# Optimization experiments

Hardware: AMD Instinct MI355X
Metric: run time of the kernel (lower is better)

Reference implementation:

```python
import jax, jax.numpy as jnp
import numpy as np

N_NODES = 100000
N_EDGES = 1600000
IN_DIM, H1, H2, OUT_DIM = 128, 64, 64, 64


def _glorot(key, shape):
    fan_in, fan_out = shape
    lim = np.sqrt(6.0 / (fan_in + fan_out)).astype(np.float32)
    return jax.random.uniform(key, shape, jnp.float32, -lim, lim)


def setup_inputs() -> dict:
    key = jax.random.key(0)
    ks = jax.random.split(key, 8)
    x = jax.random.normal(ks[0], (N_NODES, IN_DIM), jnp.float32)
    edge_index = jax.random.randint(ks[1], (2, N_EDGES), 0, N_NODES, jnp.int64)
    W1 = _glorot(ks[2], (IN_DIM, H1))
    b1 = jnp.zeros((H1,), jnp.float32)
    W2 = _glorot(ks[3], (H1, H2))
    b2 = jnp.zeros((H2,), jnp.float32)
    Wfc = _glorot(ks[4], (H2, OUT_DIM))
    bfc = jnp.zeros((OUT_DIM,), jnp.float32)
    return {"x": x, "W1": W1, "b1": b1, "W2": W2, "b2": b2,
            "Wfc": Wfc, "bfc": bfc, "edge_index": edge_index}


def _gcn_conv(x, src, dst, dinv, W, b, n_nodes):
    # PyG GCNConv: h = D^{-1/2} (A + I) D^{-1/2} (x W) + b
    h = x @ W                                   # [N, out]
    norm = dinv[src] * dinv[dst]                # [E'] edge weights
    msg = norm[:, None] * h[src]                # gather + scale, [E', out]
    agg = jax.ops.segment_sum(msg, dst, num_segments=n_nodes)
    return agg + b


def reference(x, W1, b1, W2, b2, Wfc, bfc, edge_index):
    n = x.shape[0]
    loop = jnp.arange(n, dtype=edge_index.dtype)
    src = jnp.concatenate([edge_index[0], loop])   # self-loops appended
    dst = jnp.concatenate([edge_index[1], loop])
    deg = jnp.zeros((n,), x.dtype).at[dst].add(1.0)  # degree incl. self-loop
    dinv = jax.lax.rsqrt(deg)

    h = jax.nn.relu(_gcn_conv(x, src, dst, dinv, W1, b1, n))
    h = jax.nn.relu(_gcn_conv(h, src, dst, dinv, W2, b2, n))
    embedding = h
    logits = h @ Wfc + bfc
    return embedding, logits
```

## Files before the change

kernel.cpp:

```cpp
#include <hip/hip_runtime.h>
#include <hip/hip_bf16.h>


constexpr int IN_DIM  = 128;
constexpr int HDIM    = 64;
constexpr int NBLK_A  = 256;
constexpr int BSH     = 8;
constexpr int MAXNB   = 512;
constexpr int PADSLK  = 1792;

__device__ __forceinline__ float bf2f(unsigned int u) {
    return __uint_as_float(u << 16);
}
__device__ __forceinline__ unsigned short f2bf_bits(float f) {
    __hip_bfloat16 b = __float2bfloat16(f);
    return *(unsigned short*)&b;
}


__global__ void binA_count(const int* __restrict__ dst, int* __restrict__ histg,
                           int E, int NB, int chunk) {
    __shared__ int h[MAXNB];
    for (int i = threadIdx.x; i < NB; i += 256) h[i] = 0;
    __syncthreads();
    int beg = blockIdx.x * chunk;
    int end = min(E, beg + chunk);
    for (int e = beg + threadIdx.x; e < end; e += 256)
        atomicAdd(&h[dst[e] >> BSH], 1);
    __syncthreads();
    for (int i = threadIdx.x; i < NB; i += 256)
        histg[i * NBLK_A + blockIdx.x] = h[i];
}

__global__ void binA_scanblocks(int* __restrict__ histg, int* __restrict__ btot) {
    __shared__ int sm[NBLK_A];
    int tid = threadIdx.x;
    int v = histg[blockIdx.x * NBLK_A + tid];
    sm[tid] = v;
    __syncthreads();
    for (int off = 1; off < NBLK_A; off <<= 1) {
        int t = (tid >= off) ? sm[tid - off] : 0;
        __syncthreads();
        sm[tid] += t;
        __syncthreads();
    }
    histg[blockIdx.x * NBLK_A + tid] = sm[tid] - v;
    if (tid == NBLK_A - 1) btot[blockIdx.x] = sm[tid];
}

__global__ void binA_scanbuckets(const int* __restrict__ btot, int* __restrict__ bucketbase,
                                 int NB) {
    __shared__ int sm[MAXNB];
    int tid = threadIdx.x;
    int v = (tid < NB) ? btot[tid] : 0;
    sm[tid] = v;
    __syncthreads();
    for (int off = 1; off < MAXNB; off <<= 1) {
        int t = (tid >= off) ? sm[tid - off] : 0;
        __syncthreads();
        sm[tid] += t;
        __syncthreads();
    }
    if (tid < NB) bucketbase[tid] = sm[tid] - v;
    if (tid == MAXNB - 1) bucketbase[NB] = sm[tid];
}

__global__ void binA_scatter(const int* __restrict__ src, const int* __restrict__ dst,
                             const int* __restrict__ histg, const int* __restrict__ bucketbase,
                             int* __restrict__ staging, int E, int NB, int chunk) {
    __shared__ int cur[MAXNB];
    for (int i = threadIdx.x; i < NB; i += 256)
        cur[i] = bucketbase[i] + histg[i * NBLK_A + blockIdx.x];
    __syncthreads();
    int beg = blockIdx.x * chunk;
    int end = min(E, beg + chunk);
    for (int e = beg + threadIdx.x; e < end; e += 256) {
        int s = src[e];
        int d = dst[e];
        int pos = atomicAdd(&cur[d >> BSH], 1);
        staging[pos] = (s << BSH) | (d & 255);
    }
}

__global__ void binB_finalize(const int* __restrict__ staging, const int* __restrict__ bucketbase,
                              int2* __restrict__ rows, int* __restrict__ esrc,
                              float* __restrict__ dinv, unsigned int* __restrict__ hp_rowN,
                              int N, int NB) {
    __shared__ int cnt[256], sm[256], cur[256];
    int tid = threadIdx.x;
    int b = blockIdx.x;
    int node0 = b << BSH;
    int nloc = min(256, N - node0);
    int ebeg = bucketbase[b], eend = bucketbase[b + 1];
    int ebegP = ebeg + b * PADSLK;
    cnt[tid] = 0;
    __syncthreads();
    for (int e = ebeg + tid; e < eend; e += 256)
        atomicAdd(&cnt[staging[e] & 255], 1);
    __syncthreads();
    int v = cnt[tid];
    int pv = (v + 7) & ~7;
    sm[tid] = pv;
    __syncthreads();
    for (int off = 1; off < 256; off <<= 1) {
        int t = (tid >= off) ? sm[tid - off] : 0;
        __syncthreads();
        sm[tid] += t;
        __syncthreads();
    }
    int excl = sm[tid] - pv;
    cur[tid] = excl;
    __syncthreads();
    if (tid < nloc) {
        rows[node0 + tid] = make_int2(ebegP + excl, ebegP + excl + pv);
        dinv[node0 + tid] = rsqrtf((float)v + 1.0f);
        for (int q = v; q < pv; ++q)
            esrc[ebegP + excl + q] = N;
    }
    if (b == 0 && tid < 32) hp_rowN[tid] = 0u;
    for (int e = ebeg + tid; e < eend; e += 256) {
        int p = staging[e];
        int pos = ebegP + atomicAdd(&cur[p & 255], 1);
        esrc[pos] = p >> BSH;
    }
}


template<int K, bool IBF16, bool SCALE, bool BIAS, bool OBF16>
__device__ __forceinline__ void gemm_body(
        const void* __restrict__ Xv, const float* __restrict__ W,
        const float* __restrict__ bias, const float* __restrict__ dinv,
        void* __restrict__ Yv, int n) {
    constexpr int KC = 32;
    constexpr int XSTR = 132;
    __shared__ float Xt[KC * XSTR];
    __shared__ float Ws[KC * 64];
    const int tid = threadIdx.x;
    const int node0 = blockIdx.x * 128;
    const int r0 = (tid >> 4) * 8;
    const int c0 = (tid & 15) * 4;

    float acc[8][4];
#pragma unroll
    for (int a = 0; a < 8; ++a)
#pragma unroll
        for (int b = 0; b < 4; ++b) acc[a][b] = 0.f;

    for (int kc = 0; kc < K; kc += KC) {
        __syncthreads();
#pragma unroll
        for (int i = 0; i < 4; ++i) {
            int s = tid + i * 256;
            int row = s >> 3;
            int kq = s & 7;
            int grow = node0 + row;
            float4 v = make_float4(0.f, 0.f, 0.f, 0.f);
            if (grow < n) {
                if (IBF16) {
                    uint2 u = *(const uint2*)&((const unsigned short*)Xv)[(size_t)grow * K + kc + kq * 4];
                    v.x = bf2f(u.x & 0xffff); v.y = bf2f(u.x >> 16);
                    v.z = bf2f(u.y & 0xffff); v.w = bf2f(u.y >> 16);
                } else {
                    v = *(const float4*)&((const float*)Xv)[(size_t)grow * K + kc + kq * 4];
                }
            }
            Xt[(kq * 4 + 0) * XSTR + row] = v.x;
            Xt[(kq * 4 + 1) * XSTR + row] = v.y;
            Xt[(kq * 4 + 2) * XSTR + row] = v.z;
            Xt[(kq * 4 + 3) * XSTR + row] = v.w;
        }
#pragma unroll
        for (int i = 0; i < 2; ++i) {
            int s = tid + i * 256;
            *(float4*)&Ws[s * 4] = *(const float4*)&W[(size_t)kc * 64 + s * 4];
        }
        __syncthreads();
#pragma unroll
        for (int kk = 0; kk < KC; kk += 4) {
            float4 xa[4][2];
            float4 wv[4];
#pragma unroll
            for (int i = 0; i < 4; ++i) {
                xa[i][0] = *(const float4*)&Xt[(kk + i) * XSTR + r0];
                xa[i][1] = *(const float4*)&Xt[(kk + i) * XSTR + r0 + 4];
                wv[i]    = *(const float4*)&Ws[(kk + i) * 64 + c0];
            }
#pragma unroll
            for (int i = 0; i < 4; ++i) {
                const float* xp = (const float*)&xa[i][0];
                const float* wp = (const float*)&wv[i];
#pragma unroll
                for (int rr = 0; rr < 8; ++rr)
#pragma unroll
                    for (int cc = 0; cc < 4; ++cc)
                        acc[rr][cc] += xp[rr] * wp[cc];
            }
        }
    }
#pragma unroll
    for (int rr = 0; rr < 8; ++rr) {
        int node = node0 + r0 + rr;
        if (node < n) {
            float d = SCALE ? dinv[node] : 1.0f;
            float t[4];
#pragma unroll
            for (int cc = 0; cc < 4; ++cc) {
                float v = acc[rr][cc];
                if (BIAS) v += bias[c0 + cc];
                t[cc] = v * d;
            }
            if (OBF16) {
                __hip_bfloat16 vb[4];
#pragma unroll
                for (int cc = 0; cc < 4; ++cc) vb[cc] = __float2bfloat16(t[cc]);
                *(uint2*)&((__hip_bfloat16*)Yv)[(size_t)node * 64 + c0] = *(uint2*)vb;
            } else {
                *(float4*)&((float*)Yv)[(size_t)node * 64 + c0] = *(float4*)t;
            }
        }
    }
}

__global__ __launch_bounds__(256, 4) void gemm1_kernel(
        const float* X, const float* W, const float* dinv, void* Y, int n) {
    gemm_body<IN_DIM, false, true, false, true>(X, W, nullptr, dinv, Y, n);
}
__global__ __launch_bounds__(256, 4) void gemm2_kernel(
        const void* X, const float* W, const float* dinv, void* Y, int n) {
    gemm_body<HDIM, true, true, false, true>(X, W, nullptr, dinv, Y, n);
}
__global__ __launch_bounds__(256, 4) void fc_kernel(
        const float* X, const float* W, const float* bias, void* Y, int n) {
    gemm_body<HDIM, false, false, true, false>(X, W, bias, nullptr, Y, n);
}

template<bool OBF16>
__global__ __launch_bounds__(256) void agg_kernel(
        const uint4* __restrict__ hp4, const int* __restrict__ esrc,
        const int2* __restrict__ rows, const float* __restrict__ dinv,
        const float* __restrict__ bias, void* __restrict__ out, int n) {
    const int lane = threadIdx.x & 63;
    const int j = lane & 7;
    const int node = blockIdx.x * 32 + (threadIdx.x >> 6) * 8 + (lane >> 3);
    if (node >= n) return;
    const int2 be = rows[node];

    float acc[8];
    {
        uint4 u = hp4[(size_t)node * 8 + j];
        acc[0] = bf2f(u.x & 0xffff); acc[1] = bf2f(u.x >> 16);
        acc[2] = bf2f(u.y & 0xffff); acc[3] = bf2f(u.y >> 16);
        acc[4] = bf2f(u.z & 0xffff); acc[5] = bf2f(u.z >> 16);
        acc[6] = bf2f(u.w & 0xffff); acc[7] = bf2f(u.w >> 16);
    }
    for (int k = be.x; k < be.y; k += 8) {
        int s[8];
#pragma unroll
        for (int i = 0; i < 8; ++i)
            s[i] = __builtin_nontemporal_load(&esrc[k + i]);
        uint4 u[8];
#pragma unroll
        for (int i = 0; i < 8; ++i)
            u[i] = hp4[(size_t)s[i] * 8 + j];
#pragma unroll
        for (int i = 0; i < 8; ++i) {
            acc[0] += bf2f(u[i].x & 0xffff); acc[1] += bf2f(u[i].x >> 16);
            acc[2] += bf2f(u[i].y & 0xffff); acc[3] += bf2f(u[i].y >> 16);
            acc[4] += bf2f(u[i].z & 0xffff); acc[5] += bf2f(u[i].z >> 16);
            acc[6] += bf2f(u[i].w & 0xffff); acc[7] += bf2f(u[i].w >> 16);
        }
    }
    const float d = dinv[node];
    float o[8];
#pragma unroll
    for (int t = 0; t < 8; ++t)
        o[t] = fmaxf(fmaf(d, acc[t], bias[8 * j + t]), 0.f);

    if (OBF16) {
        uint4 pk;
        pk.x = (unsigned)f2bf_bits(o[0]) | ((unsigned)f2bf_bits(o[1]) << 16);
        pk.y = (unsigned)f2bf_bits(o[2]) | ((unsigned)f2bf_bits(o[3]) << 16);
        pk.z = (unsigned)f2bf_bits(o[4]) | ((unsigned)f2bf_bits(o[5]) << 16);
        pk.w = (unsigned)f2bf_bits(o[6]) | ((unsigned)f2bf_bits(o[7]) << 16);
        ((uint4*)out)[(size_t)node * 8 + j] = pk;
    } else {
        ((float4*)out)[(size_t)node * 16 + 2 * j]     = make_float4(o[0], o[1], o[2], o[3]);
        ((float4*)out)[(size_t)node * 16 + 2 * j + 1] = make_float4(o[4], o[5], o[6], o[7]);
    }
}

extern "C" void kernel_launch(void* const* d_in, const int* in_sizes, int n_in,
                              void* d_out, int out_size, void* d_ws, size_t ws_size,
                              hipStream_t stream) {
    const float* x   = (const float*)d_in[0];
    const float* W1  = (const float*)d_in[1];
    const float* b1  = (const float*)d_in[2];
    const float* W2  = (const float*)d_in[3];
    const float* b2  = (const float*)d_in[4];
    const float* Wfc = (const float*)d_in[5];
    const float* bfc = (const float*)d_in[6];
    const int*  eidx = (const int*)d_in[7];

    const int N = in_sizes[0] / IN_DIM;
    const int E = in_sizes[7] / 2;
    const int* src = eidx;
    const int* dst = eidx + E;

    const int NB    = (N + 255) >> BSH;
    const int chunk = (E + NBLK_A - 1) / NBLK_A;
    const int EP    = E + NB * PADSLK;

    int* p = (int*)d_ws;
    int2* rows = (int2*)p;           p += (size_t)2 * N + 2;
    float* dinv = (float*)p;         p += (size_t)((N + 3) & ~3);
    int* histg = p;                  p += (size_t)((NB * NBLK_A + 3) & ~3);
    int* btot = p;                   p += 512;
    int* bucketbase = p;             p += 512;
    int* esrc = p;                   p += (size_t)((EP + 3) & ~3);
    unsigned short* hp = (unsigned short*)p;   p += (size_t)(N + 1) * 32;
    unsigned short* h1 = (unsigned short*)p;   p += (size_t)N * 32;
    int* staging = (int*)hp;
    unsigned int* hp_rowN = (unsigned int*)(hp + (size_t)N * 64);

    float* emb    = (float*)d_out;
    float* logits = emb + (size_t)N * HDIM;

    binA_count<<<NBLK_A, 256, 0, stream>>>(dst, histg, E, NB, chunk);
    binA_scanblocks<<<NB, NBLK_A, 0, stream>>>(histg, btot);
    binA_scanbuckets<<<1, MAXNB, 0, stream>>>(btot, bucketbase, NB);
    binA_scatter<<<NBLK_A, 256, 0, stream>>>(src, dst, histg, bucketbase, staging, E, NB, chunk);
    binB_finalize<<<NB, 256, 0, stream>>>(staging, bucketbase, rows, esrc, dinv, hp_rowN, N, NB);

    const int gBlocks = (N + 127) / 128;
    const int aBlocks = (N + 31) / 32;

    gemm1_kernel<<<gBlocks, 256, 0, stream>>>(x, W1, dinv, hp, N);
    agg_kernel<true><<<aBlocks, 256, 0, stream>>>(
        (const uint4*)hp, esrc, rows, dinv, b1, h1, N);

    gemm2_kernel<<<gBlocks, 256, 0, stream>>>(h1, W2, dinv, hp, N);
    agg_kernel<false><<<aBlocks, 256, 0, stream>>>(
        (const uint4*)hp, esrc, rows, dinv, b2, emb, N);

    fc_kernel<<<gBlocks, 256, 0, stream>>>(emb, Wfc, bfc, logits, N);
}
```

Baseline: 315.4 us.

## Sort nodes by padded degree class to balance aggregation wavefronts

Adds three small kernels that bucket nodes by padded edge-trip count into 16 classes and build a permutation. Both aggregation kernels then process nodes in this permuted order, so the 8 nodes sharing a wavefront have similar loop trip counts and divergence is reduced. The cost is three extra launches and an indirect perm lookup. Output writes also become scattered and lose locality with the row and hp reads.

```diff
diff --git a/kernel.cpp b/kernel.cpp
--- a/kernel.cpp
+++ b/kernel.cpp
@@ -8,6 +8,7 @@
 constexpr int BSH     = 8;
 constexpr int MAXNB   = 512;
 constexpr int PADSLK  = 1792;
+constexpr int NCLASS  = 16;
 
 __device__ __forceinline__ float bf2f(unsigned int u) {
     return __uint_as_float(u << 16);
@@ -85,7 +86,7 @@
 __global__ void binB_finalize(const int* __restrict__ staging, const int* __restrict__ bucketbase,
                               int2* __restrict__ rows, int* __restrict__ esrc,
                               float* __restrict__ dinv, unsigned int* __restrict__ hp_rowN,
-                              int N, int NB) {
+                              int* __restrict__ classCnt, int N, int NB) {
     __shared__ int cnt[256], sm[256], cur[256];
     int tid = threadIdx.x;
     int b = blockIdx.x;
@@ -94,6 +95,7 @@
     int ebeg = bucketbase[b], eend = bucketbase[b + 1];
     int ebegP = ebeg + b * PADSLK;
     cnt[tid] = 0;
+    if (b == 0 && tid < NCLASS) classCnt[tid] = 0;
     __syncthreads();
     for (int e = ebeg + tid; e < eend; e += 256)
         atomicAdd(&cnt[staging[e] & 255], 1);
@@ -123,6 +125,49 @@
         int pos = ebegP + atomicAdd(&cur[p & 255], 1);
         esrc[pos] = p >> BSH;
     }
+}
+
+
+__device__ __forceinline__ int trip_class(int2 be) {
+    return min((be.y - be.x) >> 3, NCLASS - 1);
+}
+
+__global__ void classCount(const int2* __restrict__ rows, int* __restrict__ classCnt, int N) {
+    __shared__ int lc[NCLASS];
+    if (threadIdx.x < NCLASS) lc[threadIdx.x] = 0;
+    __syncthreads();
+    int i = blockIdx.x * 256 + threadIdx.x;
+    if (i < N) atomicAdd(&lc[trip_class(rows[i])], 1);
+    __syncthreads();
+    if (threadIdx.x < NCLASS) atomicAdd(&classCnt[threadIdx.x], lc[threadIdx.x]);
+}
+
+__global__ void classScan(const int* __restrict__ classCnt, int* __restrict__ classCur) {
+    if (threadIdx.x == 0) {
+        int base = 0;
+        for (int t = 0; t < NCLASS; ++t) {
+            classCur[t] = base;
+            base += classCnt[t];
+        }
+    }
+}
+
+__global__ void classAssign(const int2* __restrict__ rows, int* __restrict__ classCur,
+                            int* __restrict__ perm, int N) {
+    __shared__ int lc[NCLASS], lbase[NCLASS];
+    if (threadIdx.x < NCLASS) lc[threadIdx.x] = 0;
+    __syncthreads();
+    int i = blockIdx.x * 256 + threadIdx.x;
+    int t = -1, r = 0;
+    if (i < N) {
+        t = trip_class(rows[i]);
+        r = atomicAdd(&lc[t], 1);
+    }
+    __syncthreads();
+    if (threadIdx.x < NCLASS && lc[threadIdx.x] > 0)
+        lbase[threadIdx.x] = atomicAdd(&classCur[threadIdx.x], lc[threadIdx.x]);
+    __syncthreads();
+    if (i < N) perm[lbase[t] + r] = i;
 }
 
 
@@ -238,11 +283,13 @@
 __global__ __launch_bounds__(256) void agg_kernel(
         const uint4* __restrict__ hp4, const int* __restrict__ esrc,
         const int2* __restrict__ rows, const float* __restrict__ dinv,
-        const float* __restrict__ bias, void* __restrict__ out, int n) {
+        const float* __restrict__ bias, const int* __restrict__ perm,
+        void* __restrict__ out, int n) {
     const int lane = threadIdx.x & 63;
     const int j = lane & 7;
-    const int node = blockIdx.x * 32 + (threadIdx.x >> 6) * 8 + (lane >> 3);
-    if (node >= n) return;
+    const int idx = blockIdx.x * 32 + (threadIdx.x >> 6) * 8 + (lane >> 3);
+    if (idx >= n) return;
+    const int node = perm[idx];
     const int2 be = rows[node];
 
     float acc[8];
@@ -316,6 +363,9 @@
     int* histg = p;                  p += (size_t)((NB * NBLK_A + 3) & ~3);
     int* btot = p;                   p += 512;
     int* bucketbase = p;             p += 512;
+    int* classCnt = p;               p += NCLASS;
+    int* classCur = p;               p += NCLASS;
+    int* perm = p;                   p += (size_t)((N + 3) & ~3);
     int* esrc = p;                   p += (size_t)((EP + 3) & ~3);
     unsigned short* hp = (unsigned short*)p;   p += (size_t)(N + 1) * 32;
     unsigned short* h1 = (unsigned short*)p;   p += (size_t)N * 32;
@@ -325,22 +375,29 @@
     float* emb    = (float*)d_out;
     float* logits = emb + (size_t)N * HDIM;
 
+    const int nBlocks256 = (N + 255) / 256;
+
     binA_count<<<NBLK_A, 256, 0, stream>>>(dst, histg, E, NB, chunk);
     binA_scanblocks<<<NB, NBLK_A, 0, stream>>>(histg, btot);
     binA_scanbuckets<<<1, MAXNB, 0, stream>>>(btot, bucketbase, NB);
     binA_scatter<<<NBLK_A, 256, 0, stream>>>(src, dst, histg, bucketbase, staging, E, NB, chunk);
-    binB_finalize<<<NB, 256, 0, stream>>>(staging, bucketbase, rows, esrc, dinv, hp_rowN, N, NB);
+    binB_finalize<<<NB, 256, 0, stream>>>(staging, bucketbase, rows, esrc, dinv, hp_rowN,
+                                          classCnt, N, NB);
+
+    classCount<<<nBlocks256, 256, 0, stream>>>(rows, classCnt, N);
+    classScan<<<1, 64, 0, stream>>>(classCnt, classCur);
+    classAssign<<<nBlocks256, 256, 0, stream>>>(rows, classCur, perm, N);
 
     const int gBlocks = (N + 127) / 128;
     const int aBlocks = (N + 31) / 32;
 
     gemm1_kernel<<<gBlocks, 256, 0, stream>>>(x, W1, dinv, hp, N);
     agg_kernel<true><<<aBlocks, 256, 0, stream>>>(
-        (const uint4*)hp, esrc, rows, dinv, b1, h1, N);
+        (const uint4*)hp, esrc, rows, dinv, b1, perm, h1, N);
 
     gemm2_kernel<<<gBlocks, 256, 0, stream>>>(h1, W2, dinv, hp, N);
     agg_kernel<false><<<aBlocks, 256, 0, stream>>>(
-        (const uint4*)hp, esrc, rows, dinv, b2, emb, N);
+        (const uint4*)hp, esrc, rows, dinv, b2, perm, emb, N);
 
     fc_kernel<<<gBlocks, 256, 0, stream>>>(emb, Wfc, bfc, logits, N);
 }
```

New measurement: 338.8 us. 7.4% more time.

## Fold bucket scan into scatter/finalize, grid-stride aggregation with 16-wide unroll

Applied to the files above, without the earlier changes.

Removes the single-block bucket-scan kernel by having every scatter and finalize block recompute the 512-entry bucket prefix scan redundantly in shared memory, which saves one launch and its dependency bubble. The aggregation kernel becomes a grid-stride loop over a fixed 2048-block grid and processes edges 16 at a time with an 8-wide tail, so more gathers are in flight per node. The redundant per-block scans add shared-memory work and barriers. The fixed grid and larger unroll may lower occupancy through higher register use.

```diff
diff --git a/kernel.cpp b/kernel.cpp
--- a/kernel.cpp
+++ b/kernel.cpp
@@ -48,29 +48,30 @@
     if (tid == NBLK_A - 1) btot[blockIdx.x] = sm[tid];
 }
 
-__global__ void binA_scanbuckets(const int* __restrict__ btot, int* __restrict__ bucketbase,
-                                 int NB) {
-    __shared__ int sm[MAXNB];
+__device__ __forceinline__ void bucket_scan(const int* __restrict__ btot,
+                                            int* bb, int NB) {
     int tid = threadIdx.x;
-    int v = (tid < NB) ? btot[tid] : 0;
-    sm[tid] = v;
+    for (int i = tid; i < MAXNB; i += 256) bb[i] = (i < NB) ? btot[i] : 0;
     __syncthreads();
     for (int off = 1; off < MAXNB; off <<= 1) {
-        int t = (tid >= off) ? sm[tid - off] : 0;
-        __syncthreads();
-        sm[tid] += t;
-        __syncthreads();
-    }
-    if (tid < NB) bucketbase[tid] = sm[tid] - v;
-    if (tid == MAXNB - 1) bucketbase[NB] = sm[tid];
+        int i0 = tid, i1 = tid + 256;
+        int t0 = (i0 >= off) ? bb[i0 - off] : 0;
+        int t1 = (i1 >= off) ? bb[i1 - off] : 0;
+        __syncthreads();
+        bb[i0] += t0;
+        bb[i1] += t1;
+        __syncthreads();
+    }
 }
 
 __global__ void binA_scatter(const int* __restrict__ src, const int* __restrict__ dst,
-                             const int* __restrict__ histg, const int* __restrict__ bucketbase,
+                             const int* __restrict__ histg, const int* __restrict__ btot,
                              int* __restrict__ staging, int E, int NB, int chunk) {
+    __shared__ int bb[MAXNB];
     __shared__ int cur[MAXNB];
+    bucket_scan(btot, bb, NB);
     for (int i = threadIdx.x; i < NB; i += 256)
-        cur[i] = bucketbase[i] + histg[i * NBLK_A + blockIdx.x];
+        cur[i] = (bb[i] - btot[i]) + histg[i * NBLK_A + blockIdx.x];
     __syncthreads();
     int beg = blockIdx.x * chunk;
     int end = min(E, beg + chunk);
@@ -82,16 +83,19 @@
     }
 }
 
-__global__ void binB_finalize(const int* __restrict__ staging, const int* __restrict__ bucketbase,
+__global__ void binB_finalize(const int* __restrict__ staging, const int* __restrict__ btot,
                               int2* __restrict__ rows, int* __restrict__ esrc,
                               float* __restrict__ dinv, unsigned int* __restrict__ hp_rowN,
                               int N, int NB) {
+    __shared__ int bb[MAXNB];
     __shared__ int cnt[256], sm[256], cur[256];
     int tid = threadIdx.x;
     int b = blockIdx.x;
+    bucket_scan(btot, bb, NB);
     int node0 = b << BSH;
     int nloc = min(256, N - node0);
-    int ebeg = bucketbase[b], eend = bucketbase[b + 1];
+    int eend = bb[b];
+    int ebeg = eend - btot[b];
     int ebegP = ebeg + b * PADSLK;
     cnt[tid] = 0;
     __syncthreads();
@@ -241,51 +245,72 @@
         const float* __restrict__ bias, void* __restrict__ out, int n) {
     const int lane = threadIdx.x & 63;
     const int j = lane & 7;
-    const int node = blockIdx.x * 32 + (threadIdx.x >> 6) * 8 + (lane >> 3);
-    if (node >= n) return;
-    const int2 be = rows[node];
-
-    float acc[8];
-    {
-        uint4 u = hp4[(size_t)node * 8 + j];
-        acc[0] = bf2f(u.x & 0xffff); acc[1] = bf2f(u.x >> 16);
-        acc[2] = bf2f(u.y & 0xffff); acc[3] = bf2f(u.y >> 16);
-        acc[4] = bf2f(u.z & 0xffff); acc[5] = bf2f(u.z >> 16);
-        acc[6] = bf2f(u.w & 0xffff); acc[7] = bf2f(u.w >> 16);
-    }
-    for (int k = be.x; k < be.y; k += 8) {
-        int s[8];
-#pragma unroll
-        for (int i = 0; i < 8; ++i)
-            s[i] = __builtin_nontemporal_load(&esrc[k + i]);
-        uint4 u[8];
-#pragma unroll
-        for (int i = 0; i < 8; ++i)
-            u[i] = hp4[(size_t)s[i] * 8 + j];
-#pragma unroll
-        for (int i = 0; i < 8; ++i) {
-            acc[0] += bf2f(u[i].x & 0xffff); acc[1] += bf2f(u[i].x >> 16);
-            acc[2] += bf2f(u[i].y & 0xffff); acc[3] += bf2f(u[i].y >> 16);
-            acc[4] += bf2f(u[i].z & 0xffff); acc[5] += bf2f(u[i].z >> 16);
-            acc[6] += bf2f(u[i].w & 0xffff); acc[7] += bf2f(u[i].w >> 16);
-        }
-    }
-    const float d = dinv[node];
-    float o[8];
-#pragma unroll
-    for (int t = 0; t < 8; ++t)
-        o[t] = fmaxf(fmaf(d, acc[t], bias[8 * j + t]), 0.f);
-
-    if (OBF16) {
-        uint4 pk;
-        pk.x = (unsigned)f2bf_bits(o[0]) | ((unsigned)f2bf_bits(o[1]) << 16);
-        pk.y = (unsigned)f2bf_bits(o[2]) | ((unsigned)f2bf_bits(o[3]) << 16);
-        pk.z = (unsigned)f2bf_bits(o[4]) | ((unsigned)f2bf_bits(o[5]) << 16);
-        pk.w = (unsigned)f2bf_bits(o[6]) | ((unsigned)f2bf_bits(o[7]) << 16);
-        ((uint4*)out)[(size_t)node * 8 + j] = pk;
-    } else {
-        ((float4*)out)[(size_t)node * 16 + 2 * j]     = make_float4(o[0], o[1], o[2], o[3]);
-        ((float4*)out)[(size_t)node * 16 + 2 * j + 1] = make_float4(o[4], o[5], o[6], o[7]);
+    const int step = gridDim.x * 32;
+    for (int idx = blockIdx.x * 32 + (threadIdx.x >> 6) * 8 + (lane >> 3);
+         idx < n; idx += step) {
+        const int node = idx;
+        const int2 be = rows[node];
+
+        float acc[8];
+        {
+            uint4 u = hp4[(size_t)node * 8 + j];
+            acc[0] = bf2f(u.x & 0xffff); acc[1] = bf2f(u.x >> 16);
+            acc[2] = bf2f(u.y & 0xffff); acc[3] = bf2f(u.y >> 16);
+            acc[4] = bf2f(u.z & 0xffff); acc[5] = bf2f(u.z >> 16);
+            acc[6] = bf2f(u.w & 0xffff); acc[7] = bf2f(u.w >> 16);
+        }
+        int k = be.x;
+        for (; k + 16 <= be.y; k += 16) {
+            int s[16];
+#pragma unroll
+            for (int i = 0; i < 16; ++i)
+                s[i] = __builtin_nontemporal_load(&esrc[k + i]);
+            uint4 u[16];
+#pragma unroll
+            for (int i = 0; i < 16; ++i)
+                u[i] = hp4[(size_t)s[i] * 8 + j];
+#pragma unroll
+            for (int i = 0; i < 16; ++i) {
+                acc[0] += bf2f(u[i].x & 0xffff); acc[1] += bf2f(u[i].x >> 16);
+                acc[2] += bf2f(u[i].y & 0xffff); acc[3] += bf2f(u[i].y >> 16);
+                acc[4] += bf2f(u[i].z & 0xffff); acc[5] += bf2f(u[i].z >> 16);
+                acc[6] += bf2f(u[i].w & 0xffff); acc[7] += bf2f(u[i].w >> 16);
+            }
+        }
+        if (k < be.y) {
+            int s[8];
+#pragma unroll
+            for (int i = 0; i < 8; ++i)
+                s[i] = __builtin_nontemporal_load(&esrc[k + i]);
+            uint4 u[8];
+#pragma unroll
+            for (int i = 0; i < 8; ++i)
+                u[i] = hp4[(size_t)s[i] * 8 + j];
+#pragma unroll
+            for (int i = 0; i < 8; ++i) {
+                acc[0] += bf2f(u[i].x & 0xffff); acc[1] += bf2f(u[i].x >> 16);
+                acc[2] += bf2f(u[i].y & 0xffff); acc[3] += bf2f(u[i].y >> 16);
+                acc[4] += bf2f(u[i].z & 0xffff); acc[5] += bf2f(u[i].z >> 16);
+                acc[6] += bf2f(u[i].w & 0xffff); acc[7] += bf2f(u[i].w >> 16);
+            }
+        }
+        const float d = dinv[node];
+        float o[8];
+#pragma unroll
+        for (int t = 0; t < 8; ++t)
+            o[t] = fmaxf(fmaf(d, acc[t], bias[8 * j + t]), 0.f);
+
+        if (OBF16) {
+            uint4 pk;
+            pk.x = (unsigned)f2bf_bits(o[0]) | ((unsigned)f2bf_bits(o[1]) << 16);
+            pk.y = (unsigned)f2bf_bits(o[2]) | ((unsigned)f2bf_bits(o[3]) << 16);
+            pk.z = (unsigned)f2bf_bits(o[4]) | ((unsigned)f2bf_bits(o[5]) << 16);
+            pk.w = (unsigned)f2bf_bits(o[6]) | ((unsigned)f2bf_bits(o[7]) << 16);
+            ((uint4*)out)[(size_t)node * 8 + j] = pk;
+        } else {
+            ((float4*)out)[(size_t)node * 16 + 2 * j]     = make_float4(o[0], o[1], o[2], o[3]);
+            ((float4*)out)[(size_t)node * 16 + 2 * j + 1] = make_float4(o[4], o[5], o[6], o[7]);
+        }
     }
 }
 
@@ -315,7 +340,6 @@
     float* dinv = (float*)p;         p += (size_t)((N + 3) & ~3);
     int* histg = p;                  p += (size_t)((NB * NBLK_A + 3) & ~3);
     int* btot = p;                   p += 512;
-    int* bucketbase = p;             p += 512;
     int* esrc = p;                   p += (size_t)((EP + 3) & ~3);
     unsigned short* hp = (unsigned short*)p;   p += (size_t)(N + 1) * 32;
     unsigned short* h1 = (unsigned short*)p;   p += (size_t)N * 32;
@@ -327,12 +351,11 @@
 
     binA_count<<<NBLK_A, 256, 0, stream>>>(dst, histg, E, NB, chunk);
     binA_scanblocks<<<NB, NBLK_A, 0, stream>>>(histg, btot);
-    binA_scanbuckets<<<1, MAXNB, 0, stream>>>(btot, bucketbase, NB);
-    binA_scatter<<<NBLK_A, 256, 0, stream>>>(src, dst, histg, bucketbase, staging, E, NB, chunk);
-    binB_finalize<<<NB, 256, 0, stream>>>(staging, bucketbase, rows, esrc, dinv, hp_rowN, N, NB);
+    binA_scatter<<<NBLK_A, 256, 0, stream>>>(src, dst, histg, btot, staging, E, NB, chunk);
+    binB_finalize<<<NB, 256, 0, stream>>>(staging, btot, rows, esrc, dinv, hp_rowN, N, NB);
 
     const int gBlocks = (N + 127) / 128;
-    const int aBlocks = (N + 31) / 32;
+    const int aBlocks = 2048;
 
     gemm1_kernel<<<gBlocks, 256, 0, stream>>>(x, W1, dinv, hp, N);
     agg_kernel<true><<<aBlocks, 256, 0, stream>>>(
```

Measured after the change: 314.8 us. No clear change (-0.2%).
